# Performance work log

Measured on AMD Instinct MI355X. Metric: run time of the kernel, lower is better.

Reference implementation:

```python
import jax, jax.numpy as jnp
import numpy as np


def setup_inputs() -> dict:
    key = jax.random.key(0)
    k1, k2, k3, k4, k5 = jax.random.split(key, 5)
    B, N, T, O, G = 32, 256, 1024, 1024, 8
    x = jax.random.normal(k1, (B, N, T), dtype=jnp.float32)
    y = jax.random.uniform(k2, (B, G), dtype=jnp.float32)  # genre mixture weights
    weight = jax.random.normal(k3, (G, O, T), dtype=jnp.float32) * (1.0 / np.sqrt(T))
    mask = jax.random.uniform(k4, (O, T), dtype=jnp.float32)
    bias = jax.random.normal(k5, (O,), dtype=jnp.float32)
    return {"x": x, "y": y, "weight": weight, "mask": mask, "bias": bias}


def reference(x, y, weight, mask, bias):
    # mask the shared weight bank: [G,O,T] * [1,O,T]
    masked_w = weight * mask[None, :, :]
    # per-sample genre-mixed weights: [B,G] x [G,O,T] -> [B,O,T]
    w_bot = jnp.einsum('bg,got->bot', y, masked_w)
    # batched masked linear: [B,N,T] x [B,O,T] -> [B,N,O], plus bias
    return jnp.einsum('bnt,bot->bno', x, w_bot) + bias
```

## Files before the change

### kernel.cpp

```cpp
#include <hip/hip_runtime.h>
#include <hip/hip_bf16.h>
#include <stdint.h>


#define B_ 32
#define N_ 256
#define T_ 1024
#define O_ 1024
#define G_ 8

#define BM 128
#define BN 128
#define BK 32

typedef __attribute__((__ext_vector_type__(8))) __bf16 bf16x8;
typedef __attribute__((__ext_vector_type__(4))) float  f32x4;

__device__ __forceinline__ unsigned short f2bf(float f) {
    union { float f; uint32_t u; } v; v.f = f;
    uint32_t u = v.u;
    uint32_t r = (u + 0x7fffu + ((u >> 16) & 1u)) >> 16;
    return (unsigned short)r;
}

__global__ __launch_bounds__(256) void mix_kernel(
    const float* __restrict__ w,
    const float* __restrict__ mask,
    const float* __restrict__ y,
    unsigned short* __restrict__ Wb)
{
    __shared__ float ys[B_ * G_];
    ys[threadIdx.x] = y[threadIdx.x];
    __syncthreads();

    const int idx = blockIdx.x * 256 + threadIdx.x;
    const int o   = idx >> 8;
    const int t4  = (idx & 255) << 2;

    const float4 m4 = *(const float4*)(mask + (size_t)o * T_ + t4);
    float4 wv[G_];
#pragma unroll
    for (int g = 0; g < G_; ++g) {
        float4 t = *(const float4*)(w + ((size_t)g * O_ + o) * T_ + t4);
        t.x *= m4.x; t.y *= m4.y; t.z *= m4.z; t.w *= m4.w;
        wv[g] = t;
    }
    unsigned short* dst = Wb + (size_t)o * T_ + t4;
#pragma unroll 4
    for (int b = 0; b < B_; ++b) {
        float ax = 0.f, ay = 0.f, az = 0.f, aw = 0.f;
#pragma unroll
        for (int g = 0; g < G_; ++g) {
            const float yv = ys[b * G_ + g];
            ax += yv * wv[g].x; ay += yv * wv[g].y;
            az += yv * wv[g].z; aw += yv * wv[g].w;
        }
        ushort4 pk;
        pk.x = f2bf(ax); pk.y = f2bf(ay); pk.z = f2bf(az); pk.w = f2bf(aw);
        *(ushort4*)(dst + (size_t)b * O_ * T_) = pk;
    }
}

__global__ __launch_bounds__(256) void cvt_kernel(
    const float* __restrict__ x, unsigned short* __restrict__ xb)
{
    const int i = blockIdx.x * 256 + threadIdx.x;
    const float4 v = ((const float4*)x)[i];
    ushort4 pk;
    pk.x = f2bf(v.x); pk.y = f2bf(v.y); pk.z = f2bf(v.z); pk.w = f2bf(v.w);
    ((ushort4*)xb)[i] = pk;
}

__device__ __forceinline__ void load16_to_lds(const unsigned short* g, unsigned short* l) {
    __builtin_amdgcn_global_load_lds(
        (const __attribute__((address_space(1))) unsigned char*)g,
        (__attribute__((address_space(3))) unsigned char*)l,
        16, 0, 0);
}

__global__ __launch_bounds__(256, 2) void gemm_kernel(
    const unsigned short* __restrict__ xb,
    const unsigned short* __restrict__ Wb,
    const float* __restrict__ bias,
    float* __restrict__ out)
{
    __shared__ __align__(16) unsigned short lA[BM * BK];
    __shared__ __align__(16) unsigned short lB[BN * BK];

    const int tn = blockIdx.x;
    const int tm = blockIdx.y;
    const int b  = blockIdx.z;

    const int tid  = threadIdx.x;
    const int lane = tid & 63;
    const int wave = tid >> 6;
    const int wm   = (wave >> 1) * 64;
    const int wn   = (wave & 1) * 64;

    const unsigned short* Ab = xb + (size_t)b * N_ * T_ + (size_t)(tm * BM) * T_;
    const unsigned short* Bb = Wb + (size_t)b * O_ * T_ + (size_t)(tn * BN) * T_;

    const int srow = tid >> 2;
    const int scol = (tid & 3) * 8;
    const unsigned short* ga0 = Ab + (size_t)srow * T_ + scol;
    const unsigned short* gb0 = Bb + (size_t)srow * T_ + scol;
    unsigned short* la_dst = lA + tid * 8;
    unsigned short* lb_dst = lB + tid * 8;

    f32x4 acc[4][4] = {};

    const int fr = lane & 15;
    const int fq = (lane >> 4) * 8;

    for (int kt = 0; kt < T_; kt += BK) {
        load16_to_lds(ga0 + kt,            la_dst);
        load16_to_lds(ga0 + 64 * T_ + kt,  la_dst + 2048);
        load16_to_lds(gb0 + kt,            lb_dst);
        load16_to_lds(gb0 + 64 * T_ + kt,  lb_dst + 2048);
        __syncthreads();

        bf16x8 afr[4], bfr[4];
#pragma unroll
        for (int i = 0; i < 4; ++i)
            afr[i] = *(const bf16x8*)(lA + (wm + i * 16 + fr) * BK + fq);
#pragma unroll
        for (int i = 0; i < 4; ++i)
            bfr[i] = *(const bf16x8*)(lB + (wn + i * 16 + fr) * BK + fq);

#pragma unroll
        for (int mi = 0; mi < 4; ++mi)
#pragma unroll
            for (int ni = 0; ni < 4; ++ni)
                acc[mi][ni] = __builtin_amdgcn_mfma_f32_16x16x32_bf16(
                    afr[mi], bfr[ni], acc[mi][ni], 0, 0, 0);
        __syncthreads();
    }

    float* outb = out + (size_t)b * N_ * O_ + (size_t)(tm * BM) * O_ + (tn * BN);
    const int cn = lane & 15;
    const int cr = (lane >> 4) * 4;
#pragma unroll
    for (int ni = 0; ni < 4; ++ni) {
        const int col = wn + ni * 16 + cn;
        const float bv = bias[tn * BN + col];
#pragma unroll
        for (int mi = 0; mi < 4; ++mi) {
#pragma unroll
            for (int r = 0; r < 4; ++r) {
                const int row = wm + mi * 16 + cr + r;
                outb[(size_t)row * O_ + col] = acc[mi][ni][r] + bv;
            }
        }
    }
}

__global__ __launch_bounds__(256) void naive_kernel(
    const float* __restrict__ x, const float* __restrict__ y,
    const float* __restrict__ w, const float* __restrict__ mask,
    const float* __restrict__ bias, float* __restrict__ out)
{
    const int oc = blockIdx.x & 3;
    const int n  = (blockIdx.x >> 2) & (N_ - 1);
    const int b  = blockIdx.x >> 10;

    __shared__ float xs[T_];
    __shared__ float ys[G_];
    const float* xrow = x + ((size_t)b * N_ + n) * T_;
    for (int i = threadIdx.x; i < T_ / 4; i += 256)
        ((float4*)xs)[i] = ((const float4*)xrow)[i];
    if (threadIdx.x < G_) ys[threadIdx.x] = y[b * G_ + threadIdx.x];
    __syncthreads();

    const int o = oc * 256 + threadIdx.x;
    float acc = 0.f;
    for (int t = 0; t < T_; t += 4) {
        const float4 m4 = *(const float4*)(mask + (size_t)o * T_ + t);
        float4 s = {0.f, 0.f, 0.f, 0.f};
#pragma unroll
        for (int g = 0; g < G_; ++g) {
            const float4 w4 = *(const float4*)(w + ((size_t)g * O_ + o) * T_ + t);
            const float yv = ys[g];
            s.x += yv * w4.x; s.y += yv * w4.y; s.z += yv * w4.z; s.w += yv * w4.w;
        }
        acc += xs[t] * m4.x * s.x + xs[t + 1] * m4.y * s.y
             + xs[t + 2] * m4.z * s.z + xs[t + 3] * m4.w * s.w;
    }
    out[((size_t)b * N_ + n) * O_ + o] = acc + bias[o];
}

extern "C" void kernel_launch(void* const* d_in, const int* in_sizes, int n_in,
                              void* d_out, int out_size, void* d_ws, size_t ws_size,
                              hipStream_t stream) {
    const float* x    = (const float*)d_in[0];
    const float* y    = (const float*)d_in[1];
    const float* w    = (const float*)d_in[2];
    const float* mask = (const float*)d_in[3];
    const float* bias = (const float*)d_in[4];
    float* out = (float*)d_out;

    const size_t wb_bytes = (size_t)B_ * O_ * T_ * sizeof(unsigned short);
    const size_t xb_bytes = (size_t)B_ * N_ * T_ * sizeof(unsigned short);

    if (ws_size >= wb_bytes + xb_bytes) {
        unsigned short* Wb = (unsigned short*)d_ws;
        unsigned short* xb = (unsigned short*)((char*)d_ws + wb_bytes);
        mix_kernel<<<O_ * T_ / 4 / 256, 256, 0, stream>>>(w, mask, y, Wb);
        cvt_kernel<<<B_ * N_ * T_ / 4 / 256, 256, 0, stream>>>(x, xb);
        dim3 grid(O_ / BN, N_ / BM, B_);
        gemm_kernel<<<grid, 256, 0, stream>>>(xb, Wb, bias, out);
    } else {
        naive_kernel<<<B_ * N_ * (O_ / 256), 256, 0, stream>>>(x, y, w, mask, bias, out);
    }
}
```

Measured before the change: 169.0 us.

## Double GEMM K-tile with XOR-swizzled LDS layout and fuse prep kernels

Raises the GEMM K tile from 32 to 64 and loads it with an XOR-swizzled chunk layout so fragment reads from LDS avoid bank conflicts. Each tile now runs two MFMA sub-steps, which halves the barriers and the loop trips per K. The weight-mixing and x-conversion kernels are merged into one launch that branches on block index, removing one launch. LDS use per block doubles, which may reduce occupancy.

```diff
diff --git a/kernel.cpp b/kernel.cpp
--- a/kernel.cpp
+++ b/kernel.cpp
@@ -11,7 +11,7 @@
 
 #define BM 128
 #define BN 128
-#define BK 32
+#define BK 64
 
 typedef __attribute__((__ext_vector_type__(8))) __bf16 bf16x8;
 typedef __attribute__((__ext_vector_type__(4))) float  f32x4;
@@ -23,52 +23,55 @@
     return (unsigned short)r;
 }
 
-__global__ __launch_bounds__(256) void mix_kernel(
+#define MIX_BLOCKS (O_ * T_ / 4 / 256)
+#define CVT_BLOCKS (B_ * N_ * T_ / 4 / 256)
+
+__global__ __launch_bounds__(256) void prep_kernel(
     const float* __restrict__ w,
     const float* __restrict__ mask,
     const float* __restrict__ y,
-    unsigned short* __restrict__ Wb)
+    const float* __restrict__ x,
+    unsigned short* __restrict__ Wb,
+    unsigned short* __restrict__ xb)
 {
-    __shared__ float ys[B_ * G_];
-    ys[threadIdx.x] = y[threadIdx.x];
-    __syncthreads();
-
-    const int idx = blockIdx.x * 256 + threadIdx.x;
-    const int o   = idx >> 8;
-    const int t4  = (idx & 255) << 2;
-
-    const float4 m4 = *(const float4*)(mask + (size_t)o * T_ + t4);
-    float4 wv[G_];
-#pragma unroll
-    for (int g = 0; g < G_; ++g) {
-        float4 t = *(const float4*)(w + ((size_t)g * O_ + o) * T_ + t4);
-        t.x *= m4.x; t.y *= m4.y; t.z *= m4.z; t.w *= m4.w;
-        wv[g] = t;
-    }
-    unsigned short* dst = Wb + (size_t)o * T_ + t4;
+    if (blockIdx.x < MIX_BLOCKS) {
+        __shared__ float ys[B_ * G_];
+        ys[threadIdx.x] = y[threadIdx.x];
+        __syncthreads();
+
+        const int idx = blockIdx.x * 256 + threadIdx.x;
+        const int o   = idx >> 8;
+        const int t4  = (idx & 255) << 2;
+
+        const float4 m4 = *(const float4*)(mask + (size_t)o * T_ + t4);
+        float4 wv[G_];
+#pragma unroll
+        for (int g = 0; g < G_; ++g) {
+            float4 t = *(const float4*)(w + ((size_t)g * O_ + o) * T_ + t4);
+            t.x *= m4.x; t.y *= m4.y; t.z *= m4.z; t.w *= m4.w;
+            wv[g] = t;
+        }
+        unsigned short* dst = Wb + (size_t)o * T_ + t4;
 #pragma unroll 4
-    for (int b = 0; b < B_; ++b) {
-        float ax = 0.f, ay = 0.f, az = 0.f, aw = 0.f;
-#pragma unroll
-        for (int g = 0; g < G_; ++g) {
-            const float yv = ys[b * G_ + g];
-            ax += yv * wv[g].x; ay += yv * wv[g].y;
-            az += yv * wv[g].z; aw += yv * wv[g].w;
-        }
+        for (int b = 0; b < B_; ++b) {
+            float ax = 0.f, ay = 0.f, az = 0.f, aw = 0.f;
+#pragma unroll
+            for (int g = 0; g < G_; ++g) {
+                const float yv = ys[b * G_ + g];
+                ax += yv * wv[g].x; ay += yv * wv[g].y;
+                az += yv * wv[g].z; aw += yv * wv[g].w;
+            }
+            ushort4 pk;
+            pk.x = f2bf(ax); pk.y = f2bf(ay); pk.z = f2bf(az); pk.w = f2bf(aw);
+            *(ushort4*)(dst + (size_t)b * O_ * T_) = pk;
+        }
+    } else {
+        const int i = (blockIdx.x - MIX_BLOCKS) * 256 + threadIdx.x;
+        const float4 v = ((const float4*)x)[i];
         ushort4 pk;
-        pk.x = f2bf(ax); pk.y = f2bf(ay); pk.z = f2bf(az); pk.w = f2bf(aw);
-        *(ushort4*)(dst + (size_t)b * O_ * T_) = pk;
-    }
-}
-
-__global__ __launch_bounds__(256) void cvt_kernel(
-    const float* __restrict__ x, unsigned short* __restrict__ xb)
-{
-    const int i = blockIdx.x * 256 + threadIdx.x;
-    const float4 v = ((const float4*)x)[i];
-    ushort4 pk;
-    pk.x = f2bf(v.x); pk.y = f2bf(v.y); pk.z = f2bf(v.z); pk.w = f2bf(v.w);
-    ((ushort4*)xb)[i] = pk;
+        pk.x = f2bf(v.x); pk.y = f2bf(v.y); pk.z = f2bf(v.z); pk.w = f2bf(v.w);
+        ((ushort4*)xb)[i] = pk;
+    }
 }
 
 __device__ __forceinline__ void load16_to_lds(const unsigned short* g, unsigned short* l) {
@@ -100,39 +103,44 @@
     const unsigned short* Ab = xb + (size_t)b * N_ * T_ + (size_t)(tm * BM) * T_;
     const unsigned short* Bb = Wb + (size_t)b * O_ * T_ + (size_t)(tn * BN) * T_;
 
-    const int srow = tid >> 2;
-    const int scol = (tid & 3) * 8;
-    const unsigned short* ga0 = Ab + (size_t)srow * T_ + scol;
-    const unsigned short* gb0 = Bb + (size_t)srow * T_ + scol;
+    const int srow   = tid >> 3;
+    const int schunk = (tid & 7) ^ (srow & 7);
+    const unsigned short* ga0 = Ab + (size_t)srow * T_ + schunk * 8;
+    const unsigned short* gb0 = Bb + (size_t)srow * T_ + schunk * 8;
     unsigned short* la_dst = lA + tid * 8;
     unsigned short* lb_dst = lB + tid * 8;
 
     f32x4 acc[4][4] = {};
 
     const int fr = lane & 15;
-    const int fq = (lane >> 4) * 8;
+    const int q  = lane >> 4;
+    const int sw = fr & 7;
 
     for (int kt = 0; kt < T_; kt += BK) {
-        load16_to_lds(ga0 + kt,            la_dst);
-        load16_to_lds(ga0 + 64 * T_ + kt,  la_dst + 2048);
-        load16_to_lds(gb0 + kt,            lb_dst);
-        load16_to_lds(gb0 + 64 * T_ + kt,  lb_dst + 2048);
+#pragma unroll
+        for (int i = 0; i < 4; ++i) {
+            load16_to_lds(ga0 + kt + (size_t)(i * 32) * T_, la_dst + i * 2048);
+            load16_to_lds(gb0 + kt + (size_t)(i * 32) * T_, lb_dst + i * 2048);
+        }
         __syncthreads();
 
-        bf16x8 afr[4], bfr[4];
-#pragma unroll
-        for (int i = 0; i < 4; ++i)
-            afr[i] = *(const bf16x8*)(lA + (wm + i * 16 + fr) * BK + fq);
-#pragma unroll
-        for (int i = 0; i < 4; ++i)
-            bfr[i] = *(const bf16x8*)(lB + (wn + i * 16 + fr) * BK + fq);
-
-#pragma unroll
-        for (int mi = 0; mi < 4; ++mi)
-#pragma unroll
-            for (int ni = 0; ni < 4; ++ni)
-                acc[mi][ni] = __builtin_amdgcn_mfma_f32_16x16x32_bf16(
-                    afr[mi], bfr[ni], acc[mi][ni], 0, 0, 0);
+#pragma unroll
+        for (int kk = 0; kk < 2; ++kk) {
+            const int cp = ((kk * 4 + q) ^ sw) * 8;
+            bf16x8 afr[4], bfr[4];
+#pragma unroll
+            for (int i = 0; i < 4; ++i)
+                afr[i] = *(const bf16x8*)(lA + (wm + i * 16 + fr) * BK + cp);
+#pragma unroll
+            for (int i = 0; i < 4; ++i)
+                bfr[i] = *(const bf16x8*)(lB + (wn + i * 16 + fr) * BK + cp);
+#pragma unroll
+            for (int mi = 0; mi < 4; ++mi)
+#pragma unroll
+                for (int ni = 0; ni < 4; ++ni)
+                    acc[mi][ni] = __builtin_amdgcn_mfma_f32_16x16x32_bf16(
+                        afr[mi], bfr[ni], acc[mi][ni], 0, 0, 0);
+        }
         __syncthreads();
     }
 
@@ -204,8 +212,7 @@
     if (ws_size >= wb_bytes + xb_bytes) {
         unsigned short* Wb = (unsigned short*)d_ws;
         unsigned short* xb = (unsigned short*)((char*)d_ws + wb_bytes);
-        mix_kernel<<<O_ * T_ / 4 / 256, 256, 0, stream>>>(w, mask, y, Wb);
-        cvt_kernel<<<B_ * N_ * T_ / 4 / 256, 256, 0, stream>>>(x, xb);
+        prep_kernel<<<MIX_BLOCKS + CVT_BLOCKS, 256, 0, stream>>>(w, mask, y, x, Wb, xb);
         dim3 grid(O_ / BN, N_ / BM, B_);
         gemm_kernel<<<grid, 256, 0, stream>>>(xb, Wb, bias, out);
     } else {
```

New measurement: 165.3 us. 2.1% less time.
